# Kernel optimization log

Measured on AMD Instinct MI355X. Metric: run time of the kernel, lower is better.

Reference implementation:

```python
import jax, jax.numpy as jnp
import numpy as np

B, S, D, H = 4, 2048, 1024, 16
DH = D // H


def setup_inputs() -> dict:
    key = jax.random.key(0)
    ks = jax.random.split(key, 12)
    inv = 1.0 / np.sqrt(D)
    inp = {
        "queries": jax.random.normal(ks[0], (B, S, D), jnp.float32),
        "keys": jax.random.normal(ks[1], (B, S, D), jnp.float32),
        "values": jax.random.normal(ks[2], (B, S, D), jnp.float32),
        # causal mask: 1.0 where attention is disallowed (strictly upper triangle)
        "mask": jnp.triu(jnp.ones((S, S), jnp.float32), k=1)[None, None, :, :],
        "Wq": jax.random.normal(ks[3], (D, D), jnp.float32) * inv,
        "bq": jnp.zeros((D,), jnp.float32),
        "Wk": jax.random.normal(ks[4], (D, D), jnp.float32) * inv,
        "bk": jnp.zeros((D,), jnp.float32),
        "Wv": jax.random.normal(ks[5], (D, D), jnp.float32) * inv,
        "bv": jnp.zeros((D,), jnp.float32),
        "Wo": jax.random.normal(ks[6], (D, D), jnp.float32) * inv,
        "bo": jnp.zeros((D,), jnp.float32),
    }
    return inp


def _split_heads(x):
    # [B, S, D] -> [B, H, S, DH]
    b, s, _ = x.shape
    return x.reshape(b, s, H, DH).transpose(0, 2, 1, 3)


def reference(queries, keys, values, mask, Wq, bq, Wk, bk, Wv, bv, Wo, bo):
    q = _split_heads(queries @ Wq + bq)
    k = _split_heads(keys @ Wk + bk)
    v = _split_heads(values @ Wv + bv)
    scores = jnp.einsum("bhqd,bhkd->bhqk", q, k) / jnp.sqrt(jnp.float32(DH))
    scores = scores + mask * -1e9
    attn = jax.nn.softmax(scores, axis=-1)
    ctx = jnp.einsum("bhqk,bhkd->bhqd", attn, v)  # [B,H,S,DH]
    ctx = ctx.transpose(0, 2, 1, 3).reshape(queries.shape[0], -1, D)
    return ctx @ Wo + bo
```

## Files before the change

kernel.cpp:

```cpp
#include <hip/hip_runtime.h>
#include <hip/hip_bf16.h>

#define S_LEN 2048
#define DMODEL 1024
#define NHEAD 16
#define DHEAD 64
#define BATCH 4
#define MTOT (BATCH * S_LEN)

typedef __attribute__((ext_vector_type(8))) short short8;
typedef __attribute__((ext_vector_type(8))) unsigned short ushort8;
typedef __attribute__((ext_vector_type(4))) unsigned short ushort4v;
typedef __attribute__((ext_vector_type(4))) float f32x4;

__device__ __forceinline__ unsigned short f2bf(float x) {
    unsigned int u = __float_as_uint(x);
    u += 0x7FFFu + ((u >> 16) & 1u);
    return (unsigned short)(u >> 16);
}

__global__ __launch_bounds__(256) void k_conv3(const float* __restrict__ s0, const float* __restrict__ s1,
                                               const float* __restrict__ s2,
                                               unsigned short* __restrict__ d0, unsigned short* __restrict__ d1,
                                               unsigned short* __restrict__ d2, int n8) {
    int i = blockIdx.x * 256 + threadIdx.x;
    if (i >= n8) return;
    const float* src = blockIdx.y == 0 ? s0 : (blockIdx.y == 1 ? s1 : s2);
    unsigned short* dst = blockIdx.y == 0 ? d0 : (blockIdx.y == 1 ? d1 : d2);
    const float4* s4 = (const float4*)src;
    float4 a = s4[(size_t)i * 2];
    float4 b = s4[(size_t)i * 2 + 1];
    ushort8 v;
    v[0] = f2bf(a.x); v[1] = f2bf(a.y); v[2] = f2bf(a.z); v[3] = f2bf(a.w);
    v[4] = f2bf(b.x); v[5] = f2bf(b.y); v[6] = f2bf(b.z); v[7] = f2bf(b.w);
    *(ushort8*)(dst + (size_t)i * 8) = v;
}

__global__ __launch_bounds__(256) void k_transpose_w(const float* __restrict__ W0, const float* __restrict__ W1,
                                                     const float* __restrict__ W2, const float* __restrict__ W3,
                                                     unsigned short* __restrict__ T0, unsigned short* __restrict__ T1,
                                                     unsigned short* __restrict__ T2, unsigned short* __restrict__ T3) {
    const float* src; unsigned short* dst;
    switch (blockIdx.z) {
        case 0: src = W0; dst = T0; break;
        case 1: src = W1; dst = T1; break;
        case 2: src = W2; dst = T2; break;
        default: src = W3; dst = T3; break;
    }
    __shared__ float t[32][33];
    int tx = threadIdx.x & 31, ty = threadIdx.x >> 5;
    int n0 = blockIdx.x * 32, k0 = blockIdx.y * 32;
#pragma unroll
    for (int i = 0; i < 32; i += 8)
        t[ty + i][tx] = src[(size_t)(k0 + ty + i) * DMODEL + n0 + tx];
    __syncthreads();
#pragma unroll
    for (int i = 0; i < 32; i += 8)
        dst[(size_t)(n0 + ty + i) * DMODEL + k0 + tx] = f2bf(t[tx][ty + i]);
}

__global__ __launch_bounds__(256) void k_gemm_qkv(const unsigned short* __restrict__ Xq,
                                                  const unsigned short* __restrict__ Xk,
                                                  const unsigned short* __restrict__ Xv,
                                                  const unsigned short* __restrict__ Tq,
                                                  const unsigned short* __restrict__ Tk,
                                                  const unsigned short* __restrict__ Tv,
                                                  const float* __restrict__ bqp, const float* __restrict__ bkp,
                                                  const float* __restrict__ bvp,
                                                  unsigned short* __restrict__ Qp, unsigned short* __restrict__ Kp,
                                                  unsigned short* __restrict__ Vt) {
    int z = blockIdx.z;
    const unsigned short* A = z == 0 ? Xq : (z == 1 ? Xk : Xv);
    const unsigned short* Bt = z == 0 ? Tq : (z == 1 ? Tk : Tv);
    const float* bias = z == 0 ? bqp : (z == 1 ? bkp : bvp);
    float alpha = z == 0 ? 0.125f : 1.0f;

    __shared__ unsigned short Al[128 * 32];
    __shared__ unsigned short Bl[128 * 32];
    int tid = threadIdx.x;
    int wid = tid >> 6, lane = tid & 63;
    int lr = lane & 15, lg = lane >> 4;
    int lin = blockIdx.y * 8 + blockIdx.x;
    int tile = (lin & 7) * 64 + (lin >> 3);
    int bm = (tile >> 3) * 128, bn = (tile & 7) * 128;
    int wm = (wid >> 1) * 64, wn = (wid & 1) * 64;

    f32x4 acc[4][4];
#pragma unroll
    for (int mt = 0; mt < 4; ++mt)
#pragma unroll
        for (int nt = 0; nt < 4; ++nt) acc[mt][nt] = (f32x4)0.0f;

    for (int k0 = 0; k0 < DMODEL; k0 += 32) {
#pragma unroll
        for (int i = 0; i < 2; ++i) {
            int c = (wid * 2 + i) * 64 + lane;
            int row = c >> 2, cc = c & 3;
            const unsigned short* ga = A + (size_t)(bm + row) * DMODEL + k0 + cc * 8;
            const unsigned short* gb = Bt + (size_t)(bn + row) * DMODEL + k0 + cc * 8;
            __builtin_amdgcn_global_load_lds((const __attribute__((address_space(1))) unsigned int*)ga,
                                             (__attribute__((address_space(3))) unsigned int*)(Al + (wid * 2 + i) * 512),
                                             16, 0, 0);
            __builtin_amdgcn_global_load_lds((const __attribute__((address_space(1))) unsigned int*)gb,
                                             (__attribute__((address_space(3))) unsigned int*)(Bl + (wid * 2 + i) * 512),
                                             16, 0, 0);
        }
        __syncthreads();
        short8 af[4], bf[4];
#pragma unroll
        for (int mt = 0; mt < 4; ++mt)
            af[mt] = *(const short8*)(Al + (wm + mt * 16 + lr) * 32 + lg * 8);
#pragma unroll
        for (int nt = 0; nt < 4; ++nt)
            bf[nt] = *(const short8*)(Bl + (wn + nt * 16 + lr) * 32 + lg * 8);
        __builtin_amdgcn_s_setprio(1);
#pragma unroll
        for (int mt = 0; mt < 4; ++mt)
#pragma unroll
            for (int nt = 0; nt < 4; ++nt)
                acc[mt][nt] = __builtin_amdgcn_mfma_f32_16x16x32_bf16(af[mt], bf[nt], acc[mt][nt], 0, 0, 0);
        __builtin_amdgcn_s_setprio(0);
        __syncthreads();
    }

#pragma unroll
    for (int nt = 0; nt < 4; ++nt) {
        int col = bn + wn + nt * 16 + lr;
        float bv = bias[col];
#pragma unroll
        for (int mt = 0; mt < 4; ++mt) {
#pragma unroll
            for (int r = 0; r < 4; ++r) {
                int row = bm + wm + mt * 16 + lg * 4 + r;
                float v = (acc[mt][nt][r] + bv) * alpha;
                if (z < 2) {
                    unsigned short* dst = z == 0 ? Qp : Kp;
                    dst[(size_t)row * DMODEL + col] = f2bf(v);
                } else {
                    int h = col >> 6, d = col & 63;
                    int b = row >> 11, s = row & 2047;
                    Vt[((size_t)(b * NHEAD + h) * DHEAD + d) * S_LEN + s] = f2bf(v);
                }
            }
        }
    }
}

__global__ __launch_bounds__(256) void k_gemm_out(const unsigned short* __restrict__ A,
                                                  const unsigned short* __restrict__ Bt,
                                                  const float* __restrict__ bias,
                                                  float* __restrict__ Cout) {
    __shared__ unsigned short Al[128 * 32];
    __shared__ unsigned short Bl[128 * 32];
    int tid = threadIdx.x;
    int wid = tid >> 6, lane = tid & 63;
    int lr = lane & 15, lg = lane >> 4;
    int lin = blockIdx.y * 8 + blockIdx.x;
    int tile = (lin & 7) * 64 + (lin >> 3);
    int bm = (tile >> 3) * 128, bn = (tile & 7) * 128;
    int wm = (wid >> 1) * 64, wn = (wid & 1) * 64;

    f32x4 acc[4][4];
#pragma unroll
    for (int mt = 0; mt < 4; ++mt)
#pragma unroll
        for (int nt = 0; nt < 4; ++nt) acc[mt][nt] = (f32x4)0.0f;

    for (int k0 = 0; k0 < DMODEL; k0 += 32) {
#pragma unroll
        for (int i = 0; i < 2; ++i) {
            int c = (wid * 2 + i) * 64 + lane;
            int row = c >> 2, cc = c & 3;
            const unsigned short* ga = A + (size_t)(bm + row) * DMODEL + k0 + cc * 8;
            const unsigned short* gb = Bt + (size_t)(bn + row) * DMODEL + k0 + cc * 8;
            __builtin_amdgcn_global_load_lds((const __attribute__((address_space(1))) unsigned int*)ga,
                                             (__attribute__((address_space(3))) unsigned int*)(Al + (wid * 2 + i) * 512),
                                             16, 0, 0);
            __builtin_amdgcn_global_load_lds((const __attribute__((address_space(1))) unsigned int*)gb,
                                             (__attribute__((address_space(3))) unsigned int*)(Bl + (wid * 2 + i) * 512),
                                             16, 0, 0);
        }
        __syncthreads();
        short8 af[4], bf[4];
#pragma unroll
        for (int mt = 0; mt < 4; ++mt)
            af[mt] = *(const short8*)(Al + (wm + mt * 16 + lr) * 32 + lg * 8);
#pragma unroll
        for (int nt = 0; nt < 4; ++nt)
            bf[nt] = *(const short8*)(Bl + (wn + nt * 16 + lr) * 32 + lg * 8);
        __builtin_amdgcn_s_setprio(1);
#pragma unroll
        for (int mt = 0; mt < 4; ++mt)
#pragma unroll
            for (int nt = 0; nt < 4; ++nt)
                acc[mt][nt] = __builtin_amdgcn_mfma_f32_16x16x32_bf16(af[mt], bf[nt], acc[mt][nt], 0, 0, 0);
        __builtin_amdgcn_s_setprio(0);
        __syncthreads();
    }

#pragma unroll
    for (int nt = 0; nt < 4; ++nt) {
        int col = bn + wn + nt * 16 + lr;
        float bv = bias[col];
#pragma unroll
        for (int mt = 0; mt < 4; ++mt)
#pragma unroll
            for (int r = 0; r < 4; ++r) {
                int row = bm + wm + mt * 16 + lg * 4 + r;
                Cout[(size_t)row * DMODEL + col] = acc[mt][nt][r] + bv;
            }
    }
}

__global__ __launch_bounds__(64, 3) void k_attn(const unsigned short* __restrict__ Qp,
                                                const unsigned short* __restrict__ Kp,
                                                const unsigned short* __restrict__ Vt,
                                                unsigned short* __restrict__ Ctx) {
    int lane = threadIdx.x & 63;
    int lr = lane & 15, lg = lane >> 4;
    int bid = blockIdx.x;
    int xcd = bid & 7;
    int j = bid >> 3;
    int bh = xcd + 8 * (j & 7);
    int qb = (S_LEN / 64 - 1) - (j >> 3);
    int b = bh >> 4, h = bh & 15;
    size_t baserow = (size_t)b * S_LEN;
    int hcol = h * DHEAD;

    short8 qf[4][2];
#pragma unroll
    for (int qt = 0; qt < 4; ++qt)
#pragma unroll
        for (int ks = 0; ks < 2; ++ks)
            qf[qt][ks] = *(const short8*)(Qp + (baserow + qb * 64 + qt * 16 + lr) * DMODEL + hcol + ks * 32 + lg * 8);

    f32x4 ctx[4][4];
#pragma unroll
    for (int dt = 0; dt < 4; ++dt)
#pragma unroll
        for (int qt = 0; qt < 4; ++qt) ctx[dt][qt] = (f32x4)0.0f;

    float mrun[4], lrun[4];
#pragma unroll
    for (int qt = 0; qt < 4; ++qt) { mrun[qt] = -1e30f; lrun[qt] = 0.0f; }

    const unsigned short* vth = Vt + (size_t)bh * DHEAD * S_LEN;

    for (int kb = 0; kb <= qb; ++kb) {
        f32x4 s[4][4];
#pragma unroll
        for (int kt = 0; kt < 4; ++kt)
#pragma unroll
            for (int qt = 0; qt < 4; ++qt) s[kt][qt] = (f32x4)0.0f;
#pragma unroll
        for (int kt = 0; kt < 4; ++kt) {
            short8 kf[2];
#pragma unroll
            for (int ks = 0; ks < 2; ++ks)
                kf[ks] = *(const short8*)(Kp + (baserow + kb * 64 + kt * 16 + lr) * DMODEL + hcol + ks * 32 + lg * 8);
            __builtin_amdgcn_s_setprio(1);
#pragma unroll
            for (int qt = 0; qt < 4; ++qt)
#pragma unroll
                for (int ks = 0; ks < 2; ++ks)
                    s[kt][qt] = __builtin_amdgcn_mfma_f32_16x16x32_bf16(kf[ks], qf[qt][ks], s[kt][qt], 0, 0, 0);
            __builtin_amdgcn_s_setprio(0);
        }

        short8 vf[4][2];
        {
            const unsigned short* vb = vth + (size_t)kb * 64 + 4 * lg;
#pragma unroll
            for (int dt = 0; dt < 4; ++dt)
#pragma unroll
                for (int ks = 0; ks < 2; ++ks) {
                    ushort4v lo = *(const ushort4v*)(vb + (size_t)(dt * 16 + lr) * S_LEN + 32 * ks);
                    ushort4v hi = *(const ushort4v*)(vb + (size_t)(dt * 16 + lr) * S_LEN + 32 * ks + 16);
                    short8 t;
                    t[0] = (short)lo[0]; t[1] = (short)lo[1]; t[2] = (short)lo[2]; t[3] = (short)lo[3];
                    t[4] = (short)hi[0]; t[5] = (short)hi[1]; t[6] = (short)hi[2]; t[7] = (short)hi[3];
                    vf[dt][ks] = t;
                }
        }

        if (kb == qb) {
#pragma unroll
            for (int kt = 0; kt < 4; ++kt)
#pragma unroll
                for (int qt = 0; qt < 4; ++qt)
#pragma unroll
                    for (int r = 0; r < 4; ++r)
                        if (kt * 16 + lg * 4 + r > qt * 16 + lr) s[kt][qt][r] = -1e30f;
        }

        short8 pf[4][2];
#pragma unroll
        for (int qt = 0; qt < 4; ++qt) {
            float mx = -1e30f;
#pragma unroll
            for (int kt = 0; kt < 4; ++kt)
#pragma unroll
                for (int r = 0; r < 4; ++r) mx = fmaxf(mx, s[kt][qt][r]);
            mx = fmaxf(mx, __shfl_xor(mx, 16));
            mx = fmaxf(mx, __shfl_xor(mx, 32));
            float mnew = fmaxf(mrun[qt], mx);
            float scale = __expf(mrun[qt] - mnew);
            mrun[qt] = mnew;
            float rs = 0.0f;
#pragma unroll
            for (int kt = 0; kt < 4; ++kt)
#pragma unroll
                for (int r = 0; r < 4; ++r) {
                    float p = __expf(s[kt][qt][r] - mnew);
                    s[kt][qt][r] = p;
                    rs += p;
                }
            rs += __shfl_xor(rs, 16);
            rs += __shfl_xor(rs, 32);
            lrun[qt] = lrun[qt] * scale + rs;
#pragma unroll
            for (int dt = 0; dt < 4; ++dt)
#pragma unroll
                for (int r = 0; r < 4; ++r) ctx[dt][qt][r] *= scale;
#pragma unroll
            for (int ks = 0; ks < 2; ++ks)
#pragma unroll
                for (int jj = 0; jj < 8; ++jj)
                    pf[qt][ks][jj] = (short)f2bf(s[2 * ks + (jj >> 2)][qt][jj & 3]);
        }

        __builtin_amdgcn_s_setprio(1);
#pragma unroll
        for (int dt = 0; dt < 4; ++dt)
#pragma unroll
            for (int ks = 0; ks < 2; ++ks)
#pragma unroll
                for (int qt = 0; qt < 4; ++qt)
                    ctx[dt][qt] = __builtin_amdgcn_mfma_f32_16x16x32_bf16(vf[dt][ks], pf[qt][ks], ctx[dt][qt], 0, 0, 0);
        __builtin_amdgcn_s_setprio(0);
    }

#pragma unroll
    for (int qt = 0; qt < 4; ++qt) {
        float inv = 1.0f / lrun[qt];
#pragma unroll
        for (int dt = 0; dt < 4; ++dt) {
            unsigned int lo = (unsigned int)f2bf(ctx[dt][qt][0] * inv) | ((unsigned int)f2bf(ctx[dt][qt][1] * inv) << 16);
            unsigned int hi = (unsigned int)f2bf(ctx[dt][qt][2] * inv) | ((unsigned int)f2bf(ctx[dt][qt][3] * inv) << 16);
            uint2 vv; vv.x = lo; vv.y = hi;
            *(uint2*)(Ctx + (baserow + qb * 64 + qt * 16 + lr) * DMODEL + hcol + dt * 16 + lg * 4) = vv;
        }
    }
}

extern "C" void kernel_launch(void* const* d_in, const int* in_sizes, int n_in,
                              void* d_out, int out_size, void* d_ws, size_t ws_size,
                              hipStream_t stream) {
    const float* q_in = (const float*)d_in[0];
    const float* k_in = (const float*)d_in[1];
    const float* v_in = (const float*)d_in[2];
    const float* Wq = (const float*)d_in[4];
    const float* bq = (const float*)d_in[5];
    const float* Wk = (const float*)d_in[6];
    const float* bk = (const float*)d_in[7];
    const float* Wv = (const float*)d_in[8];
    const float* bv = (const float*)d_in[9];
    const float* Wo = (const float*)d_in[10];
    const float* bo = (const float*)d_in[11];

    char* ws = (char*)d_ws;
    const size_t SZ_ACT = (size_t)MTOT * DMODEL * 2;
    const size_t SZ_W = (size_t)DMODEL * DMODEL * 2;
    unsigned short* Xq = (unsigned short*)(ws);
    unsigned short* Xk = (unsigned short*)(ws + SZ_ACT);
    unsigned short* Xv = (unsigned short*)(ws + 2 * SZ_ACT);
    unsigned short* Tq = (unsigned short*)(ws + 3 * SZ_ACT);
    unsigned short* Tk = (unsigned short*)(ws + 3 * SZ_ACT + SZ_W);
    unsigned short* Tv = (unsigned short*)(ws + 3 * SZ_ACT + 2 * SZ_W);
    unsigned short* To = (unsigned short*)(ws + 3 * SZ_ACT + 3 * SZ_W);
    unsigned short* Qp = (unsigned short*)(ws + 3 * SZ_ACT + 4 * SZ_W);
    unsigned short* Kp = (unsigned short*)(ws + 4 * SZ_ACT + 4 * SZ_W);
    unsigned short* Vt = (unsigned short*)(ws + 5 * SZ_ACT + 4 * SZ_W);
    unsigned short* Cx = (unsigned short*)(ws + 6 * SZ_ACT + 4 * SZ_W);

    int n8 = MTOT * DMODEL / 8;
    k_conv3<<<dim3((n8 + 255) / 256, 3), 256, 0, stream>>>(q_in, k_in, v_in, Xq, Xk, Xv, n8);
    k_transpose_w<<<dim3(32, 32, 4), 256, 0, stream>>>(Wq, Wk, Wv, Wo, Tq, Tk, Tv, To);

    k_gemm_qkv<<<dim3(8, 64, 3), 256, 0, stream>>>(Xq, Xk, Xv, Tq, Tk, Tv, bq, bk, bv, Qp, Kp, Vt);

    k_attn<<<dim3((S_LEN / 64) * BATCH * NHEAD), 64, 0, stream>>>(Qp, Kp, Vt, Cx);

    k_gemm_out<<<dim3(8, 64), 256, 0, stream>>>(Cx, To, bo, (float*)d_out);
}
```

Measured before the change: 520.1 us.

## Split attention key blocks across two waves with LDS merge, lazy rescale, exp2

The attention kernel now runs two waves per block, each handling alternate key blocks, and merges their partial softmax states through shared memory at the end. This shortens the serial per-block loop and raises parallelism. The softmax folds log2(e) into the Q scale so it can use exp2. It skips the running-max rescale unless the maximum grows by more than 8. It uses a packed bf16 conversion instruction and loads V just before the PV MFMAs. Costs are extra LDS for the merge and a sync, and the lazy rescale leaves exponentials up to 2^8 before normalisation, which affects accuracy.

```diff
diff --git a/kernel.cpp b/kernel.cpp
--- a/kernel.cpp
+++ b/kernel.cpp
@@ -11,12 +11,19 @@
 typedef __attribute__((ext_vector_type(8))) short short8;
 typedef __attribute__((ext_vector_type(8))) unsigned short ushort8;
 typedef __attribute__((ext_vector_type(4))) unsigned short ushort4v;
+typedef __attribute__((ext_vector_type(4))) unsigned int uint4v;
 typedef __attribute__((ext_vector_type(4))) float f32x4;
 
 __device__ __forceinline__ unsigned short f2bf(float x) {
     unsigned int u = __float_as_uint(x);
     u += 0x7FFFu + ((u >> 16) & 1u);
     return (unsigned short)(u >> 16);
+}
+
+__device__ __forceinline__ unsigned int cvt_pk_bf16(float lo, float hi) {
+    unsigned int r;
+    asm("v_cvt_pk_bf16_f32 %0, %1, %2" : "=v"(r) : "v"(lo), "v"(hi));
+    return r;
 }
 
 __global__ __launch_bounds__(256) void k_conv3(const float* __restrict__ s0, const float* __restrict__ s1,
@@ -73,7 +80,7 @@
     const unsigned short* A = z == 0 ? Xq : (z == 1 ? Xk : Xv);
     const unsigned short* Bt = z == 0 ? Tq : (z == 1 ? Tk : Tv);
     const float* bias = z == 0 ? bqp : (z == 1 ? bkp : bvp);
-    float alpha = z == 0 ? 0.125f : 1.0f;
+    float alpha = z == 0 ? 0.125f * 1.4426950408889634f : 1.0f;
 
     __shared__ unsigned short Al[128 * 32];
     __shared__ unsigned short Bl[128 * 32];
@@ -212,11 +219,17 @@
     }
 }
 
-__global__ __launch_bounds__(64, 3) void k_attn(const unsigned short* __restrict__ Qp,
-                                                const unsigned short* __restrict__ Kp,
-                                                const unsigned short* __restrict__ Vt,
-                                                unsigned short* __restrict__ Ctx) {
-    int lane = threadIdx.x & 63;
+__global__ __launch_bounds__(128, 4) void k_attn(const unsigned short* __restrict__ Qp,
+                                                 const unsigned short* __restrict__ Kp,
+                                                 const unsigned short* __restrict__ Vt,
+                                                 unsigned short* __restrict__ Ctx) {
+    __shared__ f32x4 cbuf[4][4][64];
+    __shared__ float mbuf[4][64];
+    __shared__ float lbuf[4][64];
+
+    int tid = threadIdx.x;
+    int wid = tid >> 6;
+    int lane = tid & 63;
     int lr = lane & 15, lg = lane >> 4;
     int bid = blockIdx.x;
     int xcd = bid & 7;
@@ -246,7 +259,7 @@
 
     const unsigned short* vth = Vt + (size_t)bh * DHEAD * S_LEN;
 
-    for (int kb = 0; kb <= qb; ++kb) {
+    for (int kb = wid; kb <= qb; kb += 2) {
         f32x4 s[4][4];
 #pragma unroll
         for (int kt = 0; kt < 4; ++kt)
@@ -267,22 +280,6 @@
             __builtin_amdgcn_s_setprio(0);
         }
 
-        short8 vf[4][2];
-        {
-            const unsigned short* vb = vth + (size_t)kb * 64 + 4 * lg;
-#pragma unroll
-            for (int dt = 0; dt < 4; ++dt)
-#pragma unroll
-                for (int ks = 0; ks < 2; ++ks) {
-                    ushort4v lo = *(const ushort4v*)(vb + (size_t)(dt * 16 + lr) * S_LEN + 32 * ks);
-                    ushort4v hi = *(const ushort4v*)(vb + (size_t)(dt * 16 + lr) * S_LEN + 32 * ks + 16);
-                    short8 t;
-                    t[0] = (short)lo[0]; t[1] = (short)lo[1]; t[2] = (short)lo[2]; t[3] = (short)lo[3];
-                    t[4] = (short)hi[0]; t[5] = (short)hi[1]; t[6] = (short)hi[2]; t[7] = (short)hi[3];
-                    vf[dt][ks] = t;
-                }
-        }
-
         if (kb == qb) {
 #pragma unroll
             for (int kt = 0; kt < 4; ++kt)
@@ -293,62 +290,100 @@
                         if (kt * 16 + lg * 4 + r > qt * 16 + lr) s[kt][qt][r] = -1e30f;
         }
 
-        short8 pf[4][2];
+        unsigned int pw[4][2][4];
 #pragma unroll
         for (int qt = 0; qt < 4; ++qt) {
-            float mx = -1e30f;
-#pragma unroll
-            for (int kt = 0; kt < 4; ++kt)
-#pragma unroll
-                for (int r = 0; r < 4; ++r) mx = fmaxf(mx, s[kt][qt][r]);
+            float m0 = fmaxf(fmaxf(s[0][qt][0], s[0][qt][1]), fmaxf(s[0][qt][2], s[0][qt][3]));
+            float m1 = fmaxf(fmaxf(s[1][qt][0], s[1][qt][1]), fmaxf(s[1][qt][2], s[1][qt][3]));
+            float m2 = fmaxf(fmaxf(s[2][qt][0], s[2][qt][1]), fmaxf(s[2][qt][2], s[2][qt][3]));
+            float m3 = fmaxf(fmaxf(s[3][qt][0], s[3][qt][1]), fmaxf(s[3][qt][2], s[3][qt][3]));
+            float mx = fmaxf(fmaxf(m0, m1), fmaxf(m2, m3));
             mx = fmaxf(mx, __shfl_xor(mx, 16));
             mx = fmaxf(mx, __shfl_xor(mx, 32));
-            float mnew = fmaxf(mrun[qt], mx);
-            float scale = __expf(mrun[qt] - mnew);
-            mrun[qt] = mnew;
-            float rs = 0.0f;
+            unsigned long long grow = __ballot(mx > mrun[qt] + 8.0f);
+            if (grow) {
+                float mnew = fmaxf(mrun[qt], mx);
+                float scale = exp2f(mrun[qt] - mnew);
+                mrun[qt] = mnew;
+                lrun[qt] *= scale;
+#pragma unroll
+                for (int dt = 0; dt < 4; ++dt)
+#pragma unroll
+                    for (int r = 0; r < 4; ++r) ctx[dt][qt][r] *= scale;
+            }
+            float m = mrun[qt];
 #pragma unroll
             for (int kt = 0; kt < 4; ++kt)
 #pragma unroll
-                for (int r = 0; r < 4; ++r) {
-                    float p = __expf(s[kt][qt][r] - mnew);
-                    s[kt][qt][r] = p;
-                    rs += p;
-                }
+                for (int r = 0; r < 4; ++r) s[kt][qt][r] = exp2f(s[kt][qt][r] - m);
+            float r0 = (s[0][qt][0] + s[0][qt][1]) + (s[0][qt][2] + s[0][qt][3]);
+            float r1 = (s[1][qt][0] + s[1][qt][1]) + (s[1][qt][2] + s[1][qt][3]);
+            float r2 = (s[2][qt][0] + s[2][qt][1]) + (s[2][qt][2] + s[2][qt][3]);
+            float r3 = (s[3][qt][0] + s[3][qt][1]) + (s[3][qt][2] + s[3][qt][3]);
+            float rs = (r0 + r1) + (r2 + r3);
             rs += __shfl_xor(rs, 16);
             rs += __shfl_xor(rs, 32);
-            lrun[qt] = lrun[qt] * scale + rs;
-#pragma unroll
-            for (int dt = 0; dt < 4; ++dt)
-#pragma unroll
-                for (int r = 0; r < 4; ++r) ctx[dt][qt][r] *= scale;
-#pragma unroll
-            for (int ks = 0; ks < 2; ++ks)
-#pragma unroll
-                for (int jj = 0; jj < 8; ++jj)
-                    pf[qt][ks][jj] = (short)f2bf(s[2 * ks + (jj >> 2)][qt][jj & 3]);
-        }
-
-        __builtin_amdgcn_s_setprio(1);
+            lrun[qt] += rs;
+#pragma unroll
+            for (int ks = 0; ks < 2; ++ks) {
+                pw[qt][ks][0] = cvt_pk_bf16(s[2 * ks][qt][0], s[2 * ks][qt][1]);
+                pw[qt][ks][1] = cvt_pk_bf16(s[2 * ks][qt][2], s[2 * ks][qt][3]);
+                pw[qt][ks][2] = cvt_pk_bf16(s[2 * ks + 1][qt][0], s[2 * ks + 1][qt][1]);
+                pw[qt][ks][3] = cvt_pk_bf16(s[2 * ks + 1][qt][2], s[2 * ks + 1][qt][3]);
+            }
+        }
+
+#pragma unroll
+        for (int dt = 0; dt < 4; ++dt) {
+            const unsigned short* vrow = vth + (size_t)(dt * 16 + lr) * S_LEN + kb * 64 + 4 * lg;
+#pragma unroll
+            for (int ks = 0; ks < 2; ++ks) {
+                ushort4v lo = *(const ushort4v*)(vrow + 32 * ks);
+                ushort4v hi = *(const ushort4v*)(vrow + 32 * ks + 16);
+                short8 vf;
+                vf[0] = (short)lo[0]; vf[1] = (short)lo[1]; vf[2] = (short)lo[2]; vf[3] = (short)lo[3];
+                vf[4] = (short)hi[0]; vf[5] = (short)hi[1]; vf[6] = (short)hi[2]; vf[7] = (short)hi[3];
+                __builtin_amdgcn_s_setprio(1);
+#pragma unroll
+                for (int qt = 0; qt < 4; ++qt) {
+                    uint4v w = {pw[qt][ks][0], pw[qt][ks][1], pw[qt][ks][2], pw[qt][ks][3]};
+                    ctx[dt][qt] = __builtin_amdgcn_mfma_f32_16x16x32_bf16(vf, __builtin_bit_cast(short8, w),
+                                                                          ctx[dt][qt], 0, 0, 0);
+                }
+                __builtin_amdgcn_s_setprio(0);
+            }
+        }
+    }
+
+    if (wid == 1) {
 #pragma unroll
         for (int dt = 0; dt < 4; ++dt)
 #pragma unroll
-            for (int ks = 0; ks < 2; ++ks)
-#pragma unroll
-                for (int qt = 0; qt < 4; ++qt)
-                    ctx[dt][qt] = __builtin_amdgcn_mfma_f32_16x16x32_bf16(vf[dt][ks], pf[qt][ks], ctx[dt][qt], 0, 0, 0);
-        __builtin_amdgcn_s_setprio(0);
-    }
-
-#pragma unroll
-    for (int qt = 0; qt < 4; ++qt) {
-        float inv = 1.0f / lrun[qt];
-#pragma unroll
-        for (int dt = 0; dt < 4; ++dt) {
-            unsigned int lo = (unsigned int)f2bf(ctx[dt][qt][0] * inv) | ((unsigned int)f2bf(ctx[dt][qt][1] * inv) << 16);
-            unsigned int hi = (unsigned int)f2bf(ctx[dt][qt][2] * inv) | ((unsigned int)f2bf(ctx[dt][qt][3] * inv) << 16);
-            uint2 vv; vv.x = lo; vv.y = hi;
-            *(uint2*)(Ctx + (baserow + qb * 64 + qt * 16 + lr) * DMODEL + hcol + dt * 16 + lg * 4) = vv;
+            for (int qt = 0; qt < 4; ++qt) cbuf[dt][qt][lane] = ctx[dt][qt];
+#pragma unroll
+        for (int qt = 0; qt < 4; ++qt) { mbuf[qt][lane] = mrun[qt]; lbuf[qt][lane] = lrun[qt]; }
+    }
+    __syncthreads();
+    if (wid == 0) {
+#pragma unroll
+        for (int qt = 0; qt < 4; ++qt) {
+            float m1 = mbuf[qt][lane], l1 = lbuf[qt][lane];
+            float mM = fmaxf(mrun[qt], m1);
+            float s0 = exp2f(mrun[qt] - mM), s1 = exp2f(m1 - mM);
+            float linv = 1.0f / (lrun[qt] * s0 + l1 * s1);
+            float f0 = s0 * linv, f1 = s1 * linv;
+#pragma unroll
+            for (int dt = 0; dt < 4; ++dt) {
+                f32x4 o1 = cbuf[dt][qt][lane];
+                float o0 = ctx[dt][qt][0] * f0 + o1[0] * f1;
+                float o1v = ctx[dt][qt][1] * f0 + o1[1] * f1;
+                float o2 = ctx[dt][qt][2] * f0 + o1[2] * f1;
+                float o3 = ctx[dt][qt][3] * f0 + o1[3] * f1;
+                unsigned int lo = (unsigned int)f2bf(o0) | ((unsigned int)f2bf(o1v) << 16);
+                unsigned int hi = (unsigned int)f2bf(o2) | ((unsigned int)f2bf(o3) << 16);
+                uint2 vv; vv.x = lo; vv.y = hi;
+                *(uint2*)(Ctx + (baserow + qb * 64 + qt * 16 + lr) * DMODEL + hcol + dt * 16 + lg * 4) = vv;
+            }
         }
     }
 }
@@ -389,7 +424,7 @@
 
     k_gemm_qkv<<<dim3(8, 64, 3), 256, 0, stream>>>(Xq, Xk, Xv, Tq, Tk, Tv, bq, bk, bv, Qp, Kp, Vt);
 
-    k_attn<<<dim3((S_LEN / 64) * BATCH * NHEAD), 64, 0, stream>>>(Qp, Kp, Vt, Cx);
+    k_attn<<<dim3((S_LEN / 64) * BATCH * NHEAD), 128, 0, stream>>>(Qp, Kp, Vt, Cx);
 
     k_gemm_out<<<dim3(8, 64), 256, 0, stream>>>(Cx, To, bo, (float*)d_out);
 }
```

After: 561.8 us. +8.0%, slower.
